# Optimization experiments

Measured on AMD Instinct MI355X. Metric: run time of the kernel, lower is better.

The kernel has to match this reference:

```python
import jax, jax.numpy as jnp
import numpy as np

B, N, D_IN, D_OUT = 8, 256, 128, 128


def setup_inputs() -> dict:
    key = jax.random.key(0)
    k1, k2, k3, k4, k5 = jax.random.split(key, 5)
    hidden = jax.random.normal(k1, (B, N, D_IN), dtype=jnp.float32)
    adj = jax.random.uniform(k2, (B, N, N), dtype=jnp.float32)
    dep_embed = jax.random.normal(k3, (B, N, N, D_IN), dtype=jnp.float32)
    weight = jax.random.normal(k4, (D_IN, D_OUT), dtype=jnp.float32) * 0.05
    bias_weight = jax.random.normal(k5, (D_OUT,), dtype=jnp.float32) * 0.05
    return {"hidden": hidden, "adj": adj, "dep_embed": dep_embed,
            "weight": weight, "bias_weight": bias_weight}


def reference(hidden, adj, dep_embed, weight, bias_weight):
    # fusion[b,p,q,d] = (hidden[b,p] + dep_embed[b,p,q]) @ W   (broadcast instead of tile)
    fusion = jnp.einsum('bpqe,ed->bpqd', hidden[:, :, None, :] + dep_embed, weight)
    # out[b,i,d] = sum_j adj[b,i,j] * fusion[b,j,i,d]   (transpose+mask+reduce fused)
    out = jnp.einsum('bij,bjid->bid', adj, fusion)
    return out + bias_weight
```

## Files before the change

### kernel.cpp

```cpp
#include <hip/hip_runtime.h>


constexpr int Bc = 8;
constexpr int Nc = 256;
constexpr int Dc = 128;

typedef float floatx4 __attribute__((ext_vector_type(4)));

__global__ __launch_bounds__(256, 2) void depgcn_kernel(
    const float* __restrict__ hidden,
    const float* __restrict__ adj,
    const float* __restrict__ dep,
    const float* __restrict__ W,
    const float* __restrict__ bias,
    float* __restrict__ out)
{
    const int bi = blockIdx.x;
    const int b  = bi >> 8;
    const int i  = bi & (Nc - 1);
    const int t  = threadIdx.x;
    const int g  = t >> 5;
    const int c  = t & 31;

    __shared__ float sAdj[Nc];
    __shared__ float sP[8][Dc];
    __shared__ float sT[Dc];
    __shared__ float sO[2][Dc];

    sAdj[t] = adj[((size_t)b * Nc + i) * Nc + t];
    __syncthreads();

    const float* depP = dep + (((size_t)b * Nc) * Nc + i) * Dc + (size_t)c * 4
                            + (size_t)(g * 32) * Nc * Dc;
    const float* hidP = hidden + ((size_t)b * Nc + g * 32) * Dc + (size_t)c * 4;

    floatx4 acc = {0.f, 0.f, 0.f, 0.f};

    #pragma unroll
    for (int jj = 0; jj < 32; jj += 4) {
        const floatx4 d0 = __builtin_nontemporal_load(
            (const floatx4*)(depP + (size_t)(jj + 0) * Nc * Dc));
        const floatx4 d1 = __builtin_nontemporal_load(
            (const floatx4*)(depP + (size_t)(jj + 1) * Nc * Dc));
        const floatx4 d2 = __builtin_nontemporal_load(
            (const floatx4*)(depP + (size_t)(jj + 2) * Nc * Dc));
        const floatx4 d3 = __builtin_nontemporal_load(
            (const floatx4*)(depP + (size_t)(jj + 3) * Nc * Dc));
        const floatx4 h0 = *(const floatx4*)(hidP + (size_t)(jj + 0) * Dc);
        const floatx4 h1 = *(const floatx4*)(hidP + (size_t)(jj + 1) * Dc);
        const floatx4 h2 = *(const floatx4*)(hidP + (size_t)(jj + 2) * Dc);
        const floatx4 h3 = *(const floatx4*)(hidP + (size_t)(jj + 3) * Dc);
        const float a0 = sAdj[g * 32 + jj + 0];
        const float a1 = sAdj[g * 32 + jj + 1];
        const float a2 = sAdj[g * 32 + jj + 2];
        const float a3 = sAdj[g * 32 + jj + 3];
        acc += a0 * (d0 + h0);
        acc += a1 * (d1 + h1);
        acc += a2 * (d2 + h2);
        acc += a3 * (d3 + h3);
    }
    *(floatx4*)&sP[g][c * 4] = acc;
    __syncthreads();

    if (t < Dc) {
        float s = 0.f;
        #pragma unroll
        for (int gg = 0; gg < 8; ++gg) s += sP[gg][t];
        sT[t] = s;
    }
    __syncthreads();

    {
        const int d = t & (Dc - 1);
        const int h = t >> 7;
        const float* wp = W + (size_t)(h * 64) * Dc + d;
        float s = 0.f;
        #pragma unroll 8
        for (int e = 0; e < 64; ++e)
            s = fmaf(sT[h * 64 + e], wp[(size_t)e * Dc], s);
        sO[h][d] = s;
    }
    __syncthreads();

    if (t < Dc)
        out[((size_t)b * Nc + i) * Dc + t] = sO[0][t] + sO[1][t] + bias[t];
}

extern "C" void kernel_launch(void* const* d_in, const int* in_sizes, int n_in,
                              void* d_out, int out_size, void* d_ws, size_t ws_size,
                              hipStream_t stream) {
    const float* hidden = (const float*)d_in[0];
    const float* adj    = (const float*)d_in[1];
    const float* dep    = (const float*)d_in[2];
    const float* W      = (const float*)d_in[3];
    const float* bias   = (const float*)d_in[4];
    float* out          = (float*)d_out;

    depgcn_kernel<<<dim3(Bc * Nc), dim3(256), 0, stream>>>(hidden, adj, dep, W, bias, out);
}
```

Baseline: 358.9 us.

## Split into contiguous-streaming partial-sum pass and reduce-plus-matmul pass

The first kernel now has each block read a contiguous slab of dep_embed (8 j-rows by 64 i-rows), so loads stream sequentially instead of striding across j with a large pitch. It writes per-j-chunk partial sums to a workspace buffer. A second kernel sums the 32 chunks per output row and applies the weight matrix and bias. This trades an extra workspace write/read (about 32 MB) and a second launch for better DRAM access locality on the 268 MB dep tensor.

```diff
diff --git a/kernel.cpp b/kernel.cpp
--- a/kernel.cpp
+++ b/kernel.cpp
@@ -4,13 +4,71 @@
 constexpr int Bc = 8;
 constexpr int Nc = 256;
 constexpr int Dc = 128;
+constexpr int JC  = 8;
+constexpr int NCH = Nc / JC;
+constexpr int ISP = 4;
+constexpr int IW  = Nc / ISP;
 
 typedef float floatx4 __attribute__((ext_vector_type(4)));
 
-__global__ __launch_bounds__(256, 2) void depgcn_kernel(
+__global__ __launch_bounds__(256) void depgcn_pass1(
     const float* __restrict__ hidden,
     const float* __restrict__ adj,
     const float* __restrict__ dep,
+    float* __restrict__ U)
+{
+    const int blk = blockIdx.x;
+    const int ih  = blk & (ISP - 1);
+    const int jc  = (blk >> 2) & (NCH - 1);
+    const int b   = blk >> 7;
+    const int t   = threadIdx.x;
+
+    const int i0 = ih * IW;
+    const int j0 = jc * JC;
+
+    __shared__ float sA[JC][IW];
+    {
+        const int idx = t * 2;
+        const int il  = idx >> 3;
+        const int jl  = idx & 7;
+        const float* ap = adj + ((size_t)b * Nc + i0 + il) * Nc + j0 + jl;
+        sA[jl][il]     = ap[0];
+        sA[jl + 1][il] = ap[1];
+    }
+    __syncthreads();
+
+    floatx4 acc[8];
+    #pragma unroll
+    for (int k = 0; k < 8; ++k) acc[k] = {0.f, 0.f, 0.f, 0.f};
+
+    const int e4 = (t & 31) * 4;
+    const int r0 = t >> 5;
+
+    const float* depBase = dep + (((size_t)(b * Nc + j0)) * Nc + i0) * Dc + t * 4;
+    const float* hidBase = hidden + ((size_t)(b * Nc + j0)) * Dc + e4;
+
+    for (int jl = 0; jl < JC; ++jl) {
+        const float* dp = depBase + (size_t)jl * Nc * Dc;
+        floatx4 d[8];
+        #pragma unroll
+        for (int k = 0; k < 8; ++k)
+            d[k] = __builtin_nontemporal_load((const floatx4*)(dp + k * 1024));
+        const floatx4 h = *(const floatx4*)(hidBase + (size_t)jl * Dc);
+        #pragma unroll
+        for (int k = 0; k < 8; ++k) {
+            const float a = sA[jl][r0 + k * 8];
+            acc[k] += a * (d[k] + h);
+        }
+    }
+
+    float* up = U + (((size_t)jc * Bc + b) * ISP + ih) * (IW * Dc) + t * 4;
+    #pragma unroll
+    for (int k = 0; k < 8; ++k)
+        *(floatx4*)(up + k * 1024) = acc[k];
+}
+
+__global__ __launch_bounds__(128) void depgcn_pass2(
+    const float* __restrict__ U,
     const float* __restrict__ W,
     const float* __restrict__ bias,
     float* __restrict__ out)
@@ -18,72 +76,26 @@
     const int bi = blockIdx.x;
     const int b  = bi >> 8;
     const int i  = bi & (Nc - 1);
+    const int ih = i >> 6;
+    const int il = i & (IW - 1);
     const int t  = threadIdx.x;
-    const int g  = t >> 5;
-    const int c  = t & 31;
 
-    __shared__ float sAdj[Nc];
-    __shared__ float sP[8][Dc];
     __shared__ float sT[Dc];
-    __shared__ float sO[2][Dc];
 
-    sAdj[t] = adj[((size_t)b * Nc + i) * Nc + t];
+    float s = 0.f;
+    const float* up = U + ((size_t)b * ISP + ih) * (IW * Dc) + (size_t)il * Dc + t;
+    #pragma unroll
+    for (int jc = 0; jc < NCH; ++jc)
+        s += up[(size_t)jc * (Bc * ISP * IW * Dc)];
+    sT[t] = s;
     __syncthreads();
 
-    const float* depP = dep + (((size_t)b * Nc) * Nc + i) * Dc + (size_t)c * 4
-                            + (size_t)(g * 32) * Nc * Dc;
-    const float* hidP = hidden + ((size_t)b * Nc + g * 32) * Dc + (size_t)c * 4;
-
-    floatx4 acc = {0.f, 0.f, 0.f, 0.f};
-
-    #pragma unroll
-    for (int jj = 0; jj < 32; jj += 4) {
-        const floatx4 d0 = __builtin_nontemporal_load(
-            (const floatx4*)(depP + (size_t)(jj + 0) * Nc * Dc));
-        const floatx4 d1 = __builtin_nontemporal_load(
-            (const floatx4*)(depP + (size_t)(jj + 1) * Nc * Dc));
-        const floatx4 d2 = __builtin_nontemporal_load(
-            (const floatx4*)(depP + (size_t)(jj + 2) * Nc * Dc));
-        const floatx4 d3 = __builtin_nontemporal_load(
-            (const floatx4*)(depP + (size_t)(jj + 3) * Nc * Dc));
-        const floatx4 h0 = *(const floatx4*)(hidP + (size_t)(jj + 0) * Dc);
-        const floatx4 h1 = *(const floatx4*)(hidP + (size_t)(jj + 1) * Dc);
-        const floatx4 h2 = *(const floatx4*)(hidP + (size_t)(jj + 2) * Dc);
-        const floatx4 h3 = *(const floatx4*)(hidP + (size_t)(jj + 3) * Dc);
-        const float a0 = sAdj[g * 32 + jj + 0];
-        const float a1 = sAdj[g * 32 + jj + 1];
-        const float a2 = sAdj[g * 32 + jj + 2];
-        const float a3 = sAdj[g * 32 + jj + 3];
-        acc += a0 * (d0 + h0);
-        acc += a1 * (d1 + h1);
-        acc += a2 * (d2 + h2);
-        acc += a3 * (d3 + h3);
-    }
-    *(floatx4*)&sP[g][c * 4] = acc;
-    __syncthreads();
-
-    if (t < Dc) {
-        float s = 0.f;
-        #pragma unroll
-        for (int gg = 0; gg < 8; ++gg) s += sP[gg][t];
-        sT[t] = s;
-    }
-    __syncthreads();
-
-    {
-        const int d = t & (Dc - 1);
-        const int h = t >> 7;
-        const float* wp = W + (size_t)(h * 64) * Dc + d;
-        float s = 0.f;
-        #pragma unroll 8
-        for (int e = 0; e < 64; ++e)
-            s = fmaf(sT[h * 64 + e], wp[(size_t)e * Dc], s);
-        sO[h][d] = s;
-    }
-    __syncthreads();
-
-    if (t < Dc)
-        out[((size_t)b * Nc + i) * Dc + t] = sO[0][t] + sO[1][t] + bias[t];
+    float o = 0.f;
+    const float* wp = W + t;
+    #pragma unroll 16
+    for (int e = 0; e < Dc; ++e)
+        o = fmaf(sT[e], wp[(size_t)e * Dc], o);
+    out[((size_t)b * Nc + i) * Dc + t] = o + bias[t];
 }
 
 extern "C" void kernel_launch(void* const* d_in, const int* in_sizes, int n_in,
@@ -95,6 +107,8 @@
     const float* W      = (const float*)d_in[3];
     const float* bias   = (const float*)d_in[4];
     float* out          = (float*)d_out;
+    float* U            = (float*)d_ws;
 
-    depgcn_kernel<<<dim3(Bc * Nc), dim3(256), 0, stream>>>(hidden, adj, dep, W, bias, out);
+    depgcn_pass1<<<dim3(Bc * NCH * ISP), dim3(256), 0, stream>>>(hidden, adj, dep, U);
+    depgcn_pass2<<<dim3(Bc * Nc), dim3(128), 0, stream>>>(U, W, bias, out);
 }
```

Measured after the change: 359.2 us. About the same (+0.1%).
